# Kernel tuning notes

Hardware: AMD Instinct MI355X
Metric: run time of the kernel (lower is better)

The kernel has to match this reference:

```python
import jax, jax.numpy as jnp
import numpy as np

N_NODES = 50000
N_EDGES = 1_000_000
N_HYPER = 1024
F_IN = 128
F_EDGE = 64


def setup_inputs() -> dict:
    key = jax.random.key(0)
    ks = jax.random.split(key, 20)
    s = 0.05
    return {
        "x": jax.random.normal(ks[0], (N_NODES, F_IN), jnp.float32),
        "edge_index": jax.random.randint(ks[1], (2, N_EDGES), 0, N_NODES, dtype=jnp.int64),
        "edge_weight": jax.random.uniform(ks[2], (N_EDGES,), jnp.float32),
        "edge_features": jax.random.normal(ks[3], (N_HYPER, F_EDGE), jnp.float32),
        "adj_e": jax.random.uniform(ks[4], (N_HYPER, N_HYPER), jnp.float32) / N_HYPER,
        "T": jax.random.uniform(ks[5], (N_NODES, N_HYPER), jnp.float32) / N_HYPER,
        # HypergraphConvLayer 1: 128 -> 64
        "W1": jax.random.normal(ks[6], (F_IN, 64), jnp.float32) * s,
        "b1": jnp.zeros((64,), jnp.float32),
        # HypergraphConvLayer 2: 64 -> 32
        "W2": jax.random.normal(ks[7], (64, 32), jnp.float32) * s,
        "b2": jnp.zeros((32,), jnp.float32),
        # GraphConvolution (CensNet-style): node 32->32, edge 64->32
        "Wn": jax.random.normal(ks[8], (32, 32), jnp.float32) * s,
        "We": jax.random.normal(ks[9], (F_EDGE, 32), jnp.float32) * s,
        "bg": jnp.zeros((32,), jnp.float32),
        # class_classifier: Linear(32,32) -> ReLU -> Linear(32,2) -> Softmax
        "Wc1": jax.random.normal(ks[10], (32, 32), jnp.float32) * s,
        "bc1": jnp.zeros((32,), jnp.float32),
        "Wc2": jax.random.normal(ks[11], (32, 2), jnp.float32) * s,
        "bc2": jnp.zeros((2,), jnp.float32),
    }


def _hconv(h, W, b, src, dst, edge_weight, num_nodes):
    # linear projection then edge-weighted scatter-add: out[dst] += w * h[src]
    h = h @ W + b
    msg = h[src] * edge_weight[:, None]          # [E, d]
    return jax.ops.segment_sum(msg, dst, num_segments=num_nodes)


def reference(x, edge_index, edge_weight, edge_features, adj_e, T,
              W1, b1, W2, b2, Wn, We, bg, Wc1, bc1, Wc2, bc2):
    n = x.shape[0]
    src, dst = edge_index[0], edge_index[1]

    h = jax.nn.relu(_hconv(x, W1, b1, src, dst, edge_weight, n))   # [N,64]
    h = jax.nn.relu(_hconv(h, W2, b2, src, dst, edge_weight, n))   # [N,32]

    # aggregate_node_features: node_features[dst] += h[src]; / num_edges
    num_edges = edge_index.shape[1]
    node_features = jax.ops.segment_sum(h[src], dst, num_segments=n) / num_edges

    # edge_conv: node linear + incidence-weighted hyperedge convolution
    edge_h = adj_e @ (edge_features @ We)                           # [NE,32]
    shared = jax.nn.relu(node_features @ Wn + T @ edge_h + bg)      # [N,32]

    # class_classifier
    c = jax.nn.relu(shared @ Wc1 + bc1)
    logits = c @ Wc2 + bc2
    return jax.nn.softmax(logits, axis=1)                           # [N,2]
```

## Files before the change

### kernel.cpp

```cpp
#include <hip/hip_runtime.h>
#include <hip/hip_bf16.h>

#define RPB 256

template<int COLS, int K>
__global__ __launch_bounds__(256) void gemm_k(
    const float* __restrict__ X, const float* __restrict__ W,
    const float* __restrict__ bias, float* __restrict__ out,
    int nrows, float scale, int relu_in)
{
    constexpr int CPT = COLS / 8;
    constexpr int KT  = 32;
    constexpr int NKT = K / KT;

    __shared__ float sx[RPB * 36];
    __shared__ float sWT[COLS * 33];

    const int tid = threadIdx.x;
    const int cg  = tid & 7;
    const int rg  = tid >> 3;
    const int r0  = blockIdx.x * RPB;

    float acc[8][CPT];
    #pragma unroll
    for (int r = 0; r < 8; ++r)
        #pragma unroll
        for (int c = 0; c < CPT; ++c) acc[r][c] = 0.f;

    for (int kt = 0; kt < NKT; ++kt) {
        #pragma unroll
        for (int j = 0; j < 8; ++j) {
            int i  = tid + j * 256;
            int r  = i >> 3;
            int k4 = i & 7;
            int gr = r0 + r; if (gr >= nrows) gr = nrows - 1;
            float4 v = *(const float4*)&X[(size_t)gr * K + kt * KT + k4 * 4];
            if (relu_in) {
                v.x = fmaxf(v.x, 0.f); v.y = fmaxf(v.y, 0.f);
                v.z = fmaxf(v.z, 0.f); v.w = fmaxf(v.w, 0.f);
            }
            if (scale != 1.f) { v.x *= scale; v.y *= scale; v.z *= scale; v.w *= scale; }
            *(float4*)&sx[r * 36 + k4 * 4] = v;
        }
        for (int i = tid; i < COLS * KT; i += 256) {
            int kl = i / COLS, c = i % COLS;
            sWT[c * 33 + kl] = W[(size_t)(kt * KT + kl) * COLS + c];
        }
        __syncthreads();

        #pragma unroll
        for (int k4 = 0; k4 < 8; ++k4) {
            float4 a[8];
            #pragma unroll
            for (int r = 0; r < 8; ++r)
                a[r] = *(const float4*)&sx[(r * 32 + rg) * 36 + k4 * 4];
            #pragma unroll
            for (int cc = 0; cc < CPT; ++cc) {
                int c = cg * CPT + cc;
                float w0 = sWT[c * 33 + k4 * 4 + 0];
                float w1 = sWT[c * 33 + k4 * 4 + 1];
                float w2 = sWT[c * 33 + k4 * 4 + 2];
                float w3 = sWT[c * 33 + k4 * 4 + 3];
                #pragma unroll
                for (int r = 0; r < 8; ++r)
                    acc[r][cc] += a[r].x * w0 + a[r].y * w1 + a[r].z * w2 + a[r].w * w3;
            }
        }
        __syncthreads();
    }

    #pragma unroll
    for (int r = 0; r < 8; ++r) {
        int row = r0 + r * 32 + rg;
        if (row < nrows) {
            #pragma unroll
            for (int cc4 = 0; cc4 < CPT / 4; ++cc4) {
                int c = cg * CPT + cc4 * 4;
                float4 o;
                o.x = acc[r][cc4 * 4 + 0] + (bias ? bias[c + 0] : 0.f);
                o.y = acc[r][cc4 * 4 + 1] + (bias ? bias[c + 1] : 0.f);
                o.z = acc[r][cc4 * 4 + 2] + (bias ? bias[c + 2] : 0.f);
                o.w = acc[r][cc4 * 4 + 3] + (bias ? bias[c + 3] : 0.f);
                *(float4*)&out[(size_t)row * COLS + c] = o;
            }
        }
    }
}

__global__ __launch_bounds__(256) void tgemm_k(
    const float* __restrict__ T, const float* __restrict__ eh,
    float* __restrict__ par, int nrows)
{
    __shared__ float sx[256 * 36];
    __shared__ float seh[32 * 36];

    const int tid  = threadIdx.x;
    const int lane = tid & 63;
    const int cg   = tid >> 6;
    const int r0   = blockIdx.x * 256;
    const int ks   = blockIdx.y * 256;

    float acc[4][8];
    #pragma unroll
    for (int r = 0; r < 4; ++r)
        #pragma unroll
        for (int j = 0; j < 8; ++j) acc[r][j] = 0.f;

    for (int kt = 0; kt < 8; ++kt) {
        int kb = ks + kt * 32;
        #pragma unroll
        for (int j = 0; j < 8; ++j) {
            int i  = tid + j * 256;
            int r  = i >> 3, k4 = i & 7;
            int gr = r0 + r; if (gr >= nrows) gr = nrows - 1;
            float4 v = *(const float4*)&T[(size_t)gr * 1024 + kb + k4 * 4];
            *(float4*)&sx[r * 36 + k4 * 4] = v;
        }
        #pragma unroll
        for (int j = 0; j < 4; ++j) {
            int ii = tid + j * 256;
            int k = ii >> 5, c = ii & 31;
            seh[c * 36 + k] = eh[(size_t)(kb + k) * 32 + c];
        }
        __syncthreads();

        #pragma unroll
        for (int k4 = 0; k4 < 8; ++k4) {
            float4 a[4];
            #pragma unroll
            for (int r = 0; r < 4; ++r)
                a[r] = *(const float4*)&sx[(lane + r * 64) * 36 + k4 * 4];
            #pragma unroll
            for (int jj = 0; jj < 8; ++jj) {
                float4 w = *(const float4*)&seh[(cg * 8 + jj) * 36 + k4 * 4];
                #pragma unroll
                for (int r = 0; r < 4; ++r)
                    acc[r][jj] += a[r].x * w.x + a[r].y * w.y
                                + a[r].z * w.z + a[r].w * w.w;
            }
        }
        __syncthreads();
    }

    float* p = par + (size_t)blockIdx.y * nrows * 32;
    #pragma unroll
    for (int r = 0; r < 4; ++r) {
        int row = r0 + lane + r * 64;
        if (row < nrows) {
            float4 o0 = make_float4(acc[r][0], acc[r][1], acc[r][2], acc[r][3]);
            float4 o1 = make_float4(acc[r][4], acc[r][5], acc[r][6], acc[r][7]);
            *(float4*)&p[(size_t)row * 32 + cg * 8]     = o0;
            *(float4*)&p[(size_t)row * 32 + cg * 8 + 4] = o1;
        }
    }
}

__global__ __launch_bounds__(256) void classify_k(
    const float* __restrict__ par, const float* __restrict__ nfw,
    const float* __restrict__ bg, const float* __restrict__ Wc1,
    const float* __restrict__ bc1, const float* __restrict__ Wc2,
    const float* __restrict__ bc2, float* __restrict__ out, int nrows)
{
    __shared__ float sWc1T[1024];
    __shared__ float sWc2[64];
    __shared__ float sb[66];

    int tid = threadIdx.x;
    for (int i = tid; i < 1024; i += 256)
        sWc1T[(i & 31) * 32 + (i >> 5)] = Wc1[i];
    if (tid < 64) sWc2[tid] = Wc2[tid];
    if (tid < 32)      sb[tid] = bc1[tid];
    else if (tid < 64) sb[tid] = bg[tid - 32];
    else if (tid < 66) sb[tid] = bc2[tid - 64];
    __syncthreads();

    int row = blockIdx.x * 256 + tid;
    if (row >= nrows) return;

    size_t stride = (size_t)nrows * 32;
    float4 sh4[8];
    #pragma unroll
    for (int i4 = 0; i4 < 8; ++i4) {
        const float* base = par + (size_t)row * 32 + i4 * 4;
        float4 v0 = *(const float4*)(base);
        float4 v1 = *(const float4*)(base + stride);
        float4 v2 = *(const float4*)(base + 2 * stride);
        float4 v3 = *(const float4*)(base + 3 * stride);
        float4 nf = *(const float4*)&nfw[(size_t)row * 32 + i4 * 4];
        float4 o;
        o.x = fmaxf(v0.x + v1.x + v2.x + v3.x + nf.x + sb[32 + i4 * 4 + 0], 0.f);
        o.y = fmaxf(v0.y + v1.y + v2.y + v3.y + nf.y + sb[32 + i4 * 4 + 1], 0.f);
        o.z = fmaxf(v0.z + v1.z + v2.z + v3.z + nf.z + sb[32 + i4 * 4 + 2], 0.f);
        o.w = fmaxf(v0.w + v1.w + v2.w + v3.w + nf.w + sb[32 + i4 * 4 + 3], 0.f);
        sh4[i4] = o;
    }

    float l0 = sb[64], l1 = sb[65];
    #pragma unroll
    for (int jj = 0; jj < 32; ++jj) {
        float s = sb[jj];
        #pragma unroll
        for (int i4 = 0; i4 < 8; ++i4) {
            float4 w4 = *(const float4*)&sWc1T[jj * 32 + i4 * 4];
            s += sh4[i4].x * w4.x + sh4[i4].y * w4.y
               + sh4[i4].z * w4.z + sh4[i4].w * w4.w;
        }
        s = fmaxf(s, 0.f);
        l0 += s * sWc2[jj * 2 + 0];
        l1 += s * sWc2[jj * 2 + 1];
    }
    float p0 = 1.f / (1.f + expf(l1 - l0));
    float p1 = 1.f / (1.f + expf(l0 - l1));
    *(float2*)&out[(size_t)row * 2] = make_float2(p0, p1);
}

__global__ void hist_k(const int* __restrict__ dst, int* __restrict__ deg, int E)
{
    int e = blockIdx.x * 256 + threadIdx.x;
    if (e < E) atomicAdd(&deg[dst[e]], 1);
}

__global__ void scan1_k(const int* __restrict__ deg, int* __restrict__ bsum, int N)
{
    __shared__ int s[256];
    int t = threadIdx.x, i = blockIdx.x * 256 + t;
    s[t] = (i < N) ? deg[i] : 0;
    __syncthreads();
    for (int off = 128; off > 0; off >>= 1) {
        if (t < off) s[t] += s[t + off];
        __syncthreads();
    }
    if (t == 0) bsum[blockIdx.x] = s[0];
}

__global__ void scan2_k(const int* __restrict__ bsum, int* __restrict__ boff,
                        int NB, int* __restrict__ rsN)
{
    if (threadIdx.x == 0 && blockIdx.x == 0) {
        int acc = 0;
        for (int b = 0; b < NB; ++b) { boff[b] = acc; acc += bsum[b]; }
        *rsN = acc;
    }
}

__global__ void scan3_k(const int* __restrict__ deg, const int* __restrict__ boff,
                        int* __restrict__ rs, int* __restrict__ cur, int N)
{
    __shared__ int s[256];
    int t = threadIdx.x, i = blockIdx.x * 256 + t;
    int v = (i < N) ? deg[i] : 0;
    s[t] = v;
    __syncthreads();
    for (int off = 1; off < 256; off <<= 1) {
        int u = (t >= off) ? s[t - off] : 0;
        __syncthreads();
        s[t] += u;
        __syncthreads();
    }
    if (i < N) {
        int ex = boff[blockIdx.x] + s[t] - v;
        rs[i] = ex;
        cur[i] = ex;
    }
}

__global__ void fill_k(const int* __restrict__ src, const int* __restrict__ dst,
                       const float* __restrict__ ew, int* __restrict__ cur,
                       int* __restrict__ esrc, float* __restrict__ ews, int E)
{
    int e = blockIdx.x * 256 + threadIdx.x;
    if (e < E) {
        int pos = atomicAdd(&cur[dst[e]], 1);
        esrc[pos] = src[e];
        ews[pos]  = ew[e];
    }
}

__global__ __launch_bounds__(256) void gather64_k(
    const float* __restrict__ hp, const int* __restrict__ esrc,
    const float* __restrict__ ews, const int* __restrict__ rs,
    float* __restrict__ outv, int N)
{
    int lane = threadIdx.x & 63;
    int sub  = lane >> 4;
    int ch   = lane & 15;
    int wid  = (blockIdx.x * blockDim.x + threadIdx.x) >> 6;
    int nw   = (gridDim.x * blockDim.x) >> 6;
    for (int n = wid; n < N; n += nw) {
        int j0 = rs[n], j1 = rs[n + 1];
        float4 acc = make_float4(0.f, 0.f, 0.f, 0.f);
        for (int j = j0; j < j1; j += 4) {
            int je = j + sub;
            bool valid = je < j1;
            int idx = valid ? je : j0;
            int s = esrc[idx];
            float w = ews[idx];
            if (!valid) w = 0.f;
            float4 v = *(const float4*)&hp[(size_t)s * 64 + ch * 4];
            acc.x += v.x * w; acc.y += v.y * w;
            acc.z += v.z * w; acc.w += v.w * w;
        }
        acc.x += __shfl_xor(acc.x, 16); acc.y += __shfl_xor(acc.y, 16);
        acc.z += __shfl_xor(acc.z, 16); acc.w += __shfl_xor(acc.w, 16);
        acc.x += __shfl_xor(acc.x, 32); acc.y += __shfl_xor(acc.y, 32);
        acc.z += __shfl_xor(acc.z, 32); acc.w += __shfl_xor(acc.w, 32);
        if (lane < 16)
            *(float4*)&outv[(size_t)n * 64 + ch * 4] = acc;
    }
}

template<bool WEIGHTED, bool RELU>
__global__ __launch_bounds__(256) void gather32_k(
    const float* __restrict__ hp, const int* __restrict__ esrc,
    const float* __restrict__ ews, const int* __restrict__ rs,
    float* __restrict__ outv, int N)
{
    int lane = threadIdx.x & 63;
    int sub  = lane >> 3;
    int ch   = lane & 7;
    int wid  = (blockIdx.x * blockDim.x + threadIdx.x) >> 6;
    int nw   = (gridDim.x * blockDim.x) >> 6;
    for (int n = wid; n < N; n += nw) {
        int j0 = rs[n], j1 = rs[n + 1];
        float4 acc = make_float4(0.f, 0.f, 0.f, 0.f);
        for (int j = j0; j < j1; j += 8) {
            int je = j + sub;
            bool valid = je < j1;
            int idx = valid ? je : j0;
            int s = esrc[idx];
            float w = WEIGHTED ? ews[idx] : 1.f;
            if (!valid) w = 0.f;
            float4 v = *(const float4*)&hp[(size_t)s * 32 + ch * 4];
            if (RELU) {
                v.x = fmaxf(v.x, 0.f); v.y = fmaxf(v.y, 0.f);
                v.z = fmaxf(v.z, 0.f); v.w = fmaxf(v.w, 0.f);
            }
            acc.x += v.x * w; acc.y += v.y * w;
            acc.z += v.z * w; acc.w += v.w * w;
        }
        acc.x += __shfl_xor(acc.x, 8);  acc.y += __shfl_xor(acc.y, 8);
        acc.z += __shfl_xor(acc.z, 8);  acc.w += __shfl_xor(acc.w, 8);
        acc.x += __shfl_xor(acc.x, 16); acc.y += __shfl_xor(acc.y, 16);
        acc.z += __shfl_xor(acc.z, 16); acc.w += __shfl_xor(acc.w, 16);
        acc.x += __shfl_xor(acc.x, 32); acc.y += __shfl_xor(acc.y, 32);
        acc.z += __shfl_xor(acc.z, 32); acc.w += __shfl_xor(acc.w, 32);
        if (lane < 8)
            *(float4*)&outv[(size_t)n * 32 + ch * 4] = acc;
    }
}

__global__ void efwe_k(const float* __restrict__ ef, const float* __restrict__ We,
                       float* __restrict__ tmp)
{
    int idx = blockIdx.x * 256 + threadIdx.x;
    int row = idx >> 5, c = idx & 31;
    float s = 0.f;
    #pragma unroll
    for (int k = 0; k < 64; ++k)
        s += ef[row * 64 + k] * We[k * 32 + c];
    tmp[row * 32 + c] = s;
}

__global__ void adjmm_k(const float* __restrict__ adj, const float* __restrict__ tmp,
                        float* __restrict__ edge_h)
{
    int kq     = blockIdx.x & 3;
    int rowblk = blockIdx.x >> 2;
    int r = rowblk * 8 + (threadIdx.x >> 5);
    int c = threadIdx.x & 31;
    float s = 0.f;
    int k0 = kq * 256;
    #pragma unroll 8
    for (int k = k0; k < k0 + 256; ++k)
        s += adj[r * 1024 + k] * tmp[k * 32 + c];
    atomicAdd(&edge_h[r * 32 + c], s);
}

extern "C" void kernel_launch(void* const* d_in, const int* in_sizes, int n_in,
                              void* d_out, int out_size, void* d_ws, size_t ws_size,
                              hipStream_t stream)
{
    const float* x   = (const float*)d_in[0];
    const int*   ei  = (const int*)  d_in[1];
    const float* ew  = (const float*)d_in[2];
    const float* ef  = (const float*)d_in[3];
    const float* adj = (const float*)d_in[4];
    const float* T   = (const float*)d_in[5];
    const float* W1  = (const float*)d_in[6];
    const float* b1  = (const float*)d_in[7];
    const float* W2  = (const float*)d_in[8];
    const float* b2  = (const float*)d_in[9];
    const float* Wn  = (const float*)d_in[10];
    const float* We  = (const float*)d_in[11];
    const float* bg  = (const float*)d_in[12];
    const float* Wc1 = (const float*)d_in[13];
    const float* bc1 = (const float*)d_in[14];
    const float* Wc2 = (const float*)d_in[15];
    const float* bc2 = (const float*)d_in[16];
    float* out = (float*)d_out;

    const int N = in_sizes[0] / 128;
    const int E = in_sizes[1] / 2;
    const int* srcIdx = ei;
    const int* dstIdx = ei + E;

    float* ws = (float*)d_ws;
    size_t o = 0;
    float* h1acc  = ws + o; o += (size_t)N * 64;
    float* h2acc  = ws + o; o += (size_t)N * 32;
    float* nfacc  = ws + o; o += (size_t)N * 32;
    float* edge_h = ws + o; o += 1024 * 32;
    float* tmp    = ws + o; o += 1024 * 32;
    float* nfw    = ws + o; o += (size_t)N * 32;
    float* par    = ws + o; o += (size_t)N * 128;
    float* h1p    = par;
    float* h2p    = par + (size_t)N * 64;
    int*   esrc   = (int*)(ws + o);   o += E;
    float* ews    = ws + o;           o += E;
    int*   deg    = (int*)(ws + o);   o += N;
    int*   rs     = (int*)(ws + o);   o += N + 1;
    int*   cur    = (int*)(ws + o);   o += N + 1;
    int*   bsum   = (int*)(ws + o);   o += 256;
    int*   boff   = (int*)(ws + o);   o += 256;

    const int NB = (N + 255) / 256;

    (void)hipMemsetAsync(deg, 0, (size_t)N * sizeof(int), stream);
    (void)hipMemsetAsync(edge_h, 0, 1024 * 32 * sizeof(float), stream);

    gemm_k<64, 128><<<NB, 256, 0, stream>>>(x, W1, b1, h1p, N, 1.f, 0);

    hist_k<<<(E + 255) / 256, 256, 0, stream>>>(dstIdx, deg, E);
    scan1_k<<<NB, 256, 0, stream>>>(deg, bsum, N);
    scan2_k<<<1, 64, 0, stream>>>(bsum, boff, NB, rs + N);
    scan3_k<<<NB, 256, 0, stream>>>(deg, boff, rs, cur, N);
    fill_k<<<(E + 255) / 256, 256, 0, stream>>>(srcIdx, dstIdx, ew, cur, esrc, ews, E);

    gather64_k<<<1024, 256, 0, stream>>>(h1p, esrc, ews, rs, h1acc, N);

    gemm_k<32, 64><<<NB, 256, 0, stream>>>(h1acc, W2, b2, h2p, N, 1.f, 1);

    gather32_k<true, false><<<1024, 256, 0, stream>>>(h2p, esrc, ews, rs, h2acc, N);

    gather32_k<false, true><<<1024, 256, 0, stream>>>(h2acc, esrc, ews, rs, nfacc, N);

    efwe_k<<<128, 256, 0, stream>>>(ef, We, tmp);
    adjmm_k<<<512, 256, 0, stream>>>(adj, tmp, edge_h);

    gemm_k<32, 32><<<NB, 256, 0, stream>>>(nfacc, Wn, nullptr, nfw, N, 1.f / (float)E, 0);

    tgemm_k<<<dim3(NB, 4), 256, 0, stream>>>(T, edge_h, par, N);

    classify_k<<<NB, 256, 0, stream>>>(par, nfw, bg, Wc1, bc1, Wc2, bc2, out, N);
}
```

Measured before the change: 826.3 us.

## Rewrite T-GEMM as per-row register kernel, parallelize scan2, unroll gathers

The T@edge_h kernel now gives each thread one row of T. It loads that row straight from global memory with float4 prefetch and broadcasts edge_h from LDS, so the T tile no longer goes through shared memory and the per-k-tile barriers are gone. The single-thread serial block-offset scan becomes a 256-thread parallel LDS scan. The gather kernels process two edges per lane per iteration to raise memory-level parallelism. The risks are strided, uncoalesced T reads (each thread reads its own 1 KB row segment) and higher register pressure from 32 accumulators plus 8 prefetched float4s, which could lower occupancy. The scan2 rewrite also assumes NB ≤ 256 (196 here).

```diff
diff --git a/kernel.cpp b/kernel.cpp
--- a/kernel.cpp
+++ b/kernel.cpp
@@ -87,71 +87,66 @@
     }
 }
 
-__global__ __launch_bounds__(256) void tgemm_k(
+__global__ __launch_bounds__(256, 4) void tgemm2_k(
     const float* __restrict__ T, const float* __restrict__ eh,
     float* __restrict__ par, int nrows)
 {
-    __shared__ float sx[256 * 36];
-    __shared__ float seh[32 * 36];
-
-    const int tid  = threadIdx.x;
-    const int lane = tid & 63;
-    const int cg   = tid >> 6;
-    const int r0   = blockIdx.x * 256;
-    const int ks   = blockIdx.y * 256;
-
-    float acc[4][8];
-    #pragma unroll
-    for (int r = 0; r < 4; ++r)
-        #pragma unroll
-        for (int j = 0; j < 8; ++j) acc[r][j] = 0.f;
-
-    for (int kt = 0; kt < 8; ++kt) {
-        int kb = ks + kt * 32;
-        #pragma unroll
-        for (int j = 0; j < 8; ++j) {
-            int i  = tid + j * 256;
-            int r  = i >> 3, k4 = i & 7;
-            int gr = r0 + r; if (gr >= nrows) gr = nrows - 1;
-            float4 v = *(const float4*)&T[(size_t)gr * 1024 + kb + k4 * 4];
-            *(float4*)&sx[r * 36 + k4 * 4] = v;
-        }
-        #pragma unroll
-        for (int j = 0; j < 4; ++j) {
-            int ii = tid + j * 256;
-            int k = ii >> 5, c = ii & 31;
-            seh[c * 36 + k] = eh[(size_t)(kb + k) * 32 + c];
-        }
-        __syncthreads();
-
-        #pragma unroll
-        for (int k4 = 0; k4 < 8; ++k4) {
-            float4 a[4];
+    __shared__ float seh[256 * 32];
+    const int tid = threadIdx.x;
+    const int ks  = blockIdx.y * 256;
+
+    #pragma unroll
+    for (int j = 0; j < 8; ++j) {
+        int i = tid + j * 256;
+        *(float4*)&seh[i * 4] = *(const float4*)&eh[(size_t)ks * 32 + (size_t)i * 4];
+    }
+    __syncthreads();
+
+    int row = blockIdx.x * 256 + tid;
+    int r   = row < nrows ? row : nrows - 1;
+    const float* Tp = T + (size_t)r * 1024 + ks;
+
+    float acc[32];
+    #pragma unroll
+    for (int c = 0; c < 32; ++c) acc[c] = 0.f;
+
+    float4 t[8];
+    #pragma unroll
+    for (int q = 0; q < 8; ++q) t[q] = *(const float4*)&Tp[q * 4];
+
+    for (int kc = 0; kc < 8; ++kc) {
+        float4 tn[8];
+        if (kc < 7) {
             #pragma unroll
-            for (int r = 0; r < 4; ++r)
-                a[r] = *(const float4*)&sx[(lane + r * 64) * 36 + k4 * 4];
+            for (int q = 0; q < 8; ++q)
+                tn[q] = *(const float4*)&Tp[(kc + 1) * 32 + q * 4];
+        }
+        #pragma unroll
+        for (int q = 0; q < 8; ++q) {
             #pragma unroll
-            for (int jj = 0; jj < 8; ++jj) {
-                float4 w = *(const float4*)&seh[(cg * 8 + jj) * 36 + k4 * 4];
+            for (int j = 0; j < 4; ++j) {
+                float a = (j == 0) ? t[q].x : (j == 1) ? t[q].y : (j == 2) ? t[q].z : t[q].w;
+                int k = kc * 32 + q * 4 + j;
                 #pragma unroll
-                for (int r = 0; r < 4; ++r)
-                    acc[r][jj] += a[r].x * w.x + a[r].y * w.y
-                                + a[r].z * w.z + a[r].w * w.w;
+                for (int c4 = 0; c4 < 8; ++c4) {
+                    float4 w = *(const float4*)&seh[k * 32 + c4 * 4];
+                    acc[c4 * 4 + 0] += a * w.x;
+                    acc[c4 * 4 + 1] += a * w.y;
+                    acc[c4 * 4 + 2] += a * w.z;
+                    acc[c4 * 4 + 3] += a * w.w;
+                }
             }
         }
-        __syncthreads();
-    }
-
-    float* p = par + (size_t)blockIdx.y * nrows * 32;
-    #pragma unroll
-    for (int r = 0; r < 4; ++r) {
-        int row = r0 + lane + r * 64;
-        if (row < nrows) {
-            float4 o0 = make_float4(acc[r][0], acc[r][1], acc[r][2], acc[r][3]);
-            float4 o1 = make_float4(acc[r][4], acc[r][5], acc[r][6], acc[r][7]);
-            *(float4*)&p[(size_t)row * 32 + cg * 8]     = o0;
-            *(float4*)&p[(size_t)row * 32 + cg * 8 + 4] = o1;
-        }
+        #pragma unroll
+        for (int q = 0; q < 8; ++q) t[q] = tn[q];
+    }
+
+    if (row < nrows) {
+        float* p = par + (size_t)blockIdx.y * nrows * 32 + (size_t)row * 32;
+        #pragma unroll
+        for (int c4 = 0; c4 < 8; ++c4)
+            *(float4*)&p[c4 * 4] = make_float4(acc[c4 * 4 + 0], acc[c4 * 4 + 1],
+                                               acc[c4 * 4 + 2], acc[c4 * 4 + 3]);
     }
 }
 
@@ -236,11 +231,19 @@
 __global__ void scan2_k(const int* __restrict__ bsum, int* __restrict__ boff,
                         int NB, int* __restrict__ rsN)
 {
-    if (threadIdx.x == 0 && blockIdx.x == 0) {
-        int acc = 0;
-        for (int b = 0; b < NB; ++b) { boff[b] = acc; acc += bsum[b]; }
-        *rsN = acc;
-    }
+    __shared__ int s[256];
+    int t = threadIdx.x;
+    int v = (t < NB) ? bsum[t] : 0;
+    s[t] = v;
+    __syncthreads();
+    for (int off = 1; off < 256; off <<= 1) {
+        int u = (t >= off) ? s[t - off] : 0;
+        __syncthreads();
+        s[t] += u;
+        __syncthreads();
+    }
+    if (t < NB) boff[t] = s[t] - v;
+    if (t == NB - 1) *rsN = s[t];
 }
 
 __global__ void scan3_k(const int* __restrict__ deg, const int* __restrict__ boff,
@@ -289,16 +292,19 @@
     for (int n = wid; n < N; n += nw) {
         int j0 = rs[n], j1 = rs[n + 1];
         float4 acc = make_float4(0.f, 0.f, 0.f, 0.f);
-        for (int j = j0; j < j1; j += 4) {
-            int je = j + sub;
-            bool valid = je < j1;
-            int idx = valid ? je : j0;
-            int s = esrc[idx];
-            float w = ews[idx];
-            if (!valid) w = 0.f;
-            float4 v = *(const float4*)&hp[(size_t)s * 64 + ch * 4];
-            acc.x += v.x * w; acc.y += v.y * w;
-            acc.z += v.z * w; acc.w += v.w * w;
+        for (int j = j0; j < j1; j += 8) {
+            int ja = j + sub, jb = j + 4 + sub;
+            bool va = ja < j1, vb = jb < j1;
+            int ia = va ? ja : j0, ib = vb ? jb : j0;
+            int sa = esrc[ia], sb2 = esrc[ib];
+            float wa = va ? ews[ia] : 0.f;
+            float wb = vb ? ews[ib] : 0.f;
+            float4 v1 = *(const float4*)&hp[(size_t)sa * 64 + ch * 4];
+            float4 v2 = *(const float4*)&hp[(size_t)sb2 * 64 + ch * 4];
+            acc.x += v1.x * wa + v2.x * wb;
+            acc.y += v1.y * wa + v2.y * wb;
+            acc.z += v1.z * wa + v2.z * wb;
+            acc.w += v1.w * wa + v2.w * wb;
         }
         acc.x += __shfl_xor(acc.x, 16); acc.y += __shfl_xor(acc.y, 16);
         acc.z += __shfl_xor(acc.z, 16); acc.w += __shfl_xor(acc.w, 16);
@@ -323,20 +329,27 @@
     for (int n = wid; n < N; n += nw) {
         int j0 = rs[n], j1 = rs[n + 1];
         float4 acc = make_float4(0.f, 0.f, 0.f, 0.f);
-        for (int j = j0; j < j1; j += 8) {
-            int je = j + sub;
-            bool valid = je < j1;
-            int idx = valid ? je : j0;
-            int s = esrc[idx];
-            float w = WEIGHTED ? ews[idx] : 1.f;
-            if (!valid) w = 0.f;
-            float4 v = *(const float4*)&hp[(size_t)s * 32 + ch * 4];
+        for (int j = j0; j < j1; j += 16) {
+            int ja = j + sub, jb = j + 8 + sub;
+            bool va = ja < j1, vb = jb < j1;
+            int ia = va ? ja : j0, ib = vb ? jb : j0;
+            int sa = esrc[ia], sb2 = esrc[ib];
+            float wa = WEIGHTED ? ews[ia] : 1.f;
+            float wb = WEIGHTED ? ews[ib] : 1.f;
+            if (!va) wa = 0.f;
+            if (!vb) wb = 0.f;
+            float4 v1 = *(const float4*)&hp[(size_t)sa * 32 + ch * 4];
+            float4 v2 = *(const float4*)&hp[(size_t)sb2 * 32 + ch * 4];
             if (RELU) {
-                v.x = fmaxf(v.x, 0.f); v.y = fmaxf(v.y, 0.f);
-                v.z = fmaxf(v.z, 0.f); v.w = fmaxf(v.w, 0.f);
+                v1.x = fmaxf(v1.x, 0.f); v1.y = fmaxf(v1.y, 0.f);
+                v1.z = fmaxf(v1.z, 0.f); v1.w = fmaxf(v1.w, 0.f);
+                v2.x = fmaxf(v2.x, 0.f); v2.y = fmaxf(v2.y, 0.f);
+                v2.z = fmaxf(v2.z, 0.f); v2.w = fmaxf(v2.w, 0.f);
             }
-            acc.x += v.x * w; acc.y += v.y * w;
-            acc.z += v.z * w; acc.w += v.w * w;
+            acc.x += v1.x * wa + v2.x * wb;
+            acc.y += v1.y * wa + v2.y * wb;
+            acc.z += v1.z * wa + v2.z * wb;
+            acc.w += v1.w * wa + v2.w * wb;
         }
         acc.x += __shfl_xor(acc.x, 8);  acc.y += __shfl_xor(acc.y, 8);
         acc.z += __shfl_xor(acc.z, 8);  acc.w += __shfl_xor(acc.w, 8);
@@ -432,7 +445,7 @@
 
     hist_k<<<(E + 255) / 256, 256, 0, stream>>>(dstIdx, deg, E);
     scan1_k<<<NB, 256, 0, stream>>>(deg, bsum, N);
-    scan2_k<<<1, 64, 0, stream>>>(bsum, boff, NB, rs + N);
+    scan2_k<<<1, 256, 0, stream>>>(bsum, boff, NB, rs + N);
     scan3_k<<<NB, 256, 0, stream>>>(deg, boff, rs, cur, N);
     fill_k<<<(E + 255) / 256, 256, 0, stream>>>(srcIdx, dstIdx, ew, cur, esrc, ews, E);
 
@@ -449,7 +462,7 @@
 
     gemm_k<32, 32><<<NB, 256, 0, stream>>>(nfacc, Wn, nullptr, nfw, N, 1.f / (float)E, 0);
 
-    tgemm_k<<<dim3(NB, 4), 256, 0, stream>>>(T, edge_h, par, N);
+    tgemm2_k<<<dim3(NB, 4), 256, 0, stream>>>(T, edge_h, par, N);
 
     classify_k<<<NB, 256, 0, stream>>>(par, nfw, bg, Wc1, bc1, Wc2, bc2, out, N);
 }
```

Result: faster. 745.6 us (-9.8%).
